# Kernel tuning notes

Hardware: AMD Instinct MI355X
Metric: run time of the kernel (lower is better)

## Reference

```python
import jax, jax.numpy as jnp
import numpy as np

DIM = 2048
HEAD = 256
SEQ = 4096

def setup_inputs() -> dict:
    key = jax.random.key(0)
    ks = jax.random.split(key, 7)
    s = 1.0 / np.sqrt(DIM)
    return {
        "marketStateBatch": jax.random.normal(ks[0], (SEQ, DIM), dtype=jnp.float32),
        "Wq": jax.random.uniform(ks[1], (HEAD, DIM), jnp.float32, -s, s),
        "bq": jax.random.uniform(ks[2], (HEAD,), jnp.float32, -s, s),
        "Wk": jax.random.uniform(ks[3], (HEAD, DIM), jnp.float32, -s, s),
        "bk": jax.random.uniform(ks[4], (HEAD,), jnp.float32, -s, s),
        "Wv": jax.random.uniform(ks[5], (HEAD, DIM), jnp.float32, -s, s),
        "bv": jax.random.uniform(ks[6], (HEAD,), jnp.float32, -s, s),
    }

def reference(marketStateBatch, Wq, bq, Wk, bk, Wv, bv):
    x = marketStateBatch  # [S, D]
    q = x @ Wq.T + bq     # [S, H]
    k = x @ Wk.T + bk     # [S, H]
    v = x @ Wv.T + bv     # [S, H]
    # NOTE: original scales by sqrt(dimensionSize), the INPUT dim, not head dim.
    scores = (q @ k.T) * (1.0 / np.sqrt(DIM))  # [S, S]
    S = x.shape[0]
    causal = jnp.tril(jnp.ones((S, S), dtype=bool))
    scores = jnp.where(causal, scores, -jnp.inf)
    attn = jax.nn.softmax(scores, axis=-1)
    # torch.nan_to_num(attn, 0.0): rows are never all -inf here (diag kept),
    # but replicate the op faithfully.
    attn = jnp.nan_to_num(attn, nan=0.0)
    return attn @ v  # [S, H]
```

## Files before the change

kernel.cpp:

```cpp
#include <hip/hip_runtime.h>
#include <stdint.h>

#define SEQ 4096
#define DIMK 2048
#define HD 256

typedef __attribute__((ext_vector_type(8))) short bf16x8;
typedef __attribute__((ext_vector_type(4))) short u16x4;
typedef __attribute__((ext_vector_type(4))) float f32x4;
typedef __attribute__((ext_vector_type(16))) float f32x16;
typedef unsigned short u16;
typedef unsigned int u32;

#define BAR() asm volatile("s_barrier" ::: "memory")
#define VMCNT(n) asm volatile("s_waitcnt vmcnt(" #n ")" ::: "memory")

__device__ __forceinline__ u16 f2bf(float f) {
    u32 u = __float_as_uint(f);
    u += 0x7FFFu + ((u >> 16) & 1u);
    return (u16)(u >> 16);
}

__device__ __forceinline__ float bf2f(u16 h) {
    u32 u = ((u32)h) << 16;
    return __uint_as_float(u);
}

__device__ __forceinline__ bf16x8 pack8(f32x4 a0, f32x4 a1) {
    bf16x8 v8;
    v8[0]=(short)f2bf(a0[0]); v8[1]=(short)f2bf(a0[1]);
    v8[2]=(short)f2bf(a0[2]); v8[3]=(short)f2bf(a0[3]);
    v8[4]=(short)f2bf(a1[0]); v8[5]=(short)f2bf(a1[1]);
    v8[6]=(short)f2bf(a1[2]); v8[7]=(short)f2bf(a1[3]);
    return v8;
}

__device__ __forceinline__ void gl16(const void* g, void* l) {
    __builtin_amdgcn_global_load_lds(
        (const __attribute__((address_space(1))) void*)g,
        (__attribute__((address_space(3))) void*)l, 16, 0, 0);
}

__device__ __forceinline__ u32 cvtpk(float lo, float hi) {
    u32 d;
    asm("v_cvt_pk_bf16_f32 %0, %1, %2" : "=v"(d) : "v"(lo), "v"(hi));
    return d;
}

__device__ __forceinline__ void plswap(u32& x, u32& y) {
#if __has_builtin(__builtin_amdgcn_permlane32_swap)
    typedef int i32x2 __attribute__((ext_vector_type(2)));
    i32x2 r = __builtin_amdgcn_permlane32_swap((int)x, (int)y, false, false);
    x = (u32)r[0]; y = (u32)r[1];
#else
    asm("v_permlane32_swap_b32 %0, %1" : "+v"(x), "+v"(y));
#endif
}

__global__ __launch_bounds__(256) void cvt_all2(
    const float* __restrict__ x, const float* __restrict__ Wq,
    const float* __restrict__ Wk, const float* __restrict__ Wv,
    u16* __restrict__ xb_sw, u16* __restrict__ wb_sw)
{
    const int y = blockIdx.y;
    int i = blockIdx.x * 256 + threadIdx.x;
    int stride = gridDim.x * 256;
    if (y == 0) {
        for (; i < SEQ*DIMK/8; i += stride) {
            int row = i >> 8, c8 = i & 255;
            f32x4 a0 = *(const f32x4*)(x + (size_t)row*DIMK + c8*8);
            f32x4 a1 = *(const f32x4*)(x + (size_t)row*DIMK + c8*8 + 4);
            int mt = row >> 6, rl = row & 63, kt = c8 >> 3, sl = c8 & 7;
            size_t dst = ((size_t)(mt*32 + kt))*4096 + rl*64 + ((sl ^ (rl&7))*8);
            *(bf16x8*)(xb_sw + dst) = pack8(a0, a1);
        }
    } else {
        const float* W = (y==1) ? Wq : (y==2) ? Wk : Wv;
        for (; i < HD*DIMK/8; i += stride) {
            int row = i >> 8, c8 = i & 255;
            f32x4 a0 = *(const f32x4*)(W + (size_t)row*DIMK + c8*8);
            f32x4 a1 = *(const f32x4*)(W + (size_t)row*DIMK + c8*8 + 4);
            int gr = (y-1)*256 + row;
            int nt = gr >> 7, rl = gr & 127, kt = c8 >> 3, sl = c8 & 7;
            size_t dst = ((size_t)(nt*32 + kt))*8192 + rl*64 + ((sl ^ (rl&7))*8);
            *(bf16x8*)(wb_sw + dst) = pack8(a0, a1);
        }
    }
}

__global__ __launch_bounds__(256, 2) void qkv_gemm2b(
    const u16* __restrict__ xb_sw, const u16* __restrict__ wb_sw,
    const float* __restrict__ bq, const float* __restrict__ bk,
    const float* __restrict__ bv,
    u16* __restrict__ qb, u16* __restrict__ kb_t, u16* __restrict__ vt_t)
{
    __shared__ char T[3][24576];

    const int tid = threadIdx.x;
    const int lane = tid & 63;
    const int w = tid >> 6;
    const int r = lane & 15, g = lane >> 4;
    const int wr = w >> 1, wc = w & 1;
    const int mt = blockIdx.x;
    const int y  = blockIdx.y;
    const int z  = y >> 1;
    const float* bias = (z==0) ? bq : (z==1) ? bk : bv;

    const u16* abase = xb_sw + (size_t)mt*32*4096;
    const u16* bbase = wb_sw + (size_t)y*32*8192;

    f32x4 zero = {0.f,0.f,0.f,0.f};
    f32x4 acc[2][4];
    #pragma unroll
    for (int m = 0; m < 2; ++m)
        #pragma unroll
        for (int n = 0; n < 4; ++n) acc[m][n] = zero;

    auto stage = [&](int b, int kt) {
        const u16* ag = abase + (size_t)kt*4096 + w*1024 + lane*8;
        const u16* bg = bbase + (size_t)kt*8192 + w*2048 + lane*8;
        char* al = T[b] + w*2048;
        char* bl = T[b] + 8192 + w*4096;
        gl16(ag,        al);
        gl16(ag + 512,  al + 1024);
        gl16(bg,        bl);
        gl16(bg + 512,  bl + 1024);
        gl16(bg + 1024, bl + 2048);
        gl16(bg + 1536, bl + 3072);
    };

    stage(0, 0);
    stage(1, 1);

    for (int kt = 0; kt < 32; ++kt) {
        if (kt < 31) { VMCNT(6); } else { VMCNT(0); }
        BAR();
        if (kt + 2 < 32) stage((kt + 2) % 3, kt + 2);
        const char* A = T[kt % 3];
        const char* B = T[kt % 3] + 8192;
        __builtin_amdgcn_s_setprio(1);
        #pragma unroll
        for (int kc = 0; kc < 2; ++kc) {
            bf16x8 af[2], bfr[4];
            #pragma unroll
            for (int m = 0; m < 2; ++m) {
                int arow = wr*32 + m*16 + r;
                af[m] = *(const bf16x8*)(A + arow*128 + (((kc*4+g) ^ (arow&7)) << 4));
            }
            #pragma unroll
            for (int n = 0; n < 4; ++n) {
                int brow = wc*64 + n*16 + r;
                bfr[n] = *(const bf16x8*)(B + brow*128 + (((kc*4+g) ^ (brow&7)) << 4));
            }
            #pragma unroll
            for (int m = 0; m < 2; ++m)
                #pragma unroll
                for (int n = 0; n < 4; ++n)
                    acc[m][n] = __builtin_amdgcn_mfma_f32_16x16x32_bf16(
                        af[m], bfr[n], acc[m][n], 0, 0, 0);
        }
        __builtin_amdgcn_s_setprio(0);
    }

    const int m0 = mt*64, n0 = y*128;
    const float qs = 0.03187936f;
    if (z == 0) {
        #pragma unroll
        for (int n = 0; n < 4; ++n) {
            int hc = (n0 + wc*64 + n*16 + r) & 255;
            float bcol = bias[hc];
            #pragma unroll
            for (int m = 0; m < 2; ++m) {
                int row0 = m0 + wr*32 + m*16 + g*4;
                #pragma unroll
                for (int j = 0; j < 4; ++j)
                    qb[(size_t)(row0+j)*HD + hc] = f2bf((acc[m][n][j] + bcol) * qs);
            }
        }
    } else if (z == 1) {
        #pragma unroll
        for (int n = 0; n < 4; ++n) {
            int hc = (n0 + wc*64 + n*16 + r) & 255;
            float bcol = bias[hc];
            #pragma unroll
            for (int m = 0; m < 2; ++m) {
                int row0 = m0 + wr*32 + m*16 + g*4;
                #pragma unroll
                for (int j = 0; j < 4; ++j) {
                    int rowj = row0 + j;
                    int t = rowj >> 5, rl = rowj & 31;
                    kb_t[(size_t)t*8192 + rl*256 + (((hc>>3) ^ (rl&7))*8) + (hc&7)]
                        = f2bf(acc[m][n][j] + bcol);
                }
            }
        }
    } else {
        #pragma unroll
        for (int n = 0; n < 4; ++n) {
            int hc = (n0 + wc*64 + n*16 + r) & 255;
            float bcol = bias[hc];
            #pragma unroll
            for (int m = 0; m < 2; ++m) {
                int kv0 = m0 + wr*32 + m*16 + g*4;
                int t = kv0 >> 5, kl = kv0 & 31;
                u16x4 pk;
                #pragma unroll
                for (int j = 0; j < 4; ++j) pk[j] = (short)f2bf(acc[m][n][j] + bcol);
                *(u16x4*)(vt_t + (size_t)t*8192 + hc*32 +
                          (((kl>>3) ^ (hc&3) ^ ((hc>>2)&3))*8) + (kl&7)) = pk;
            }
        }
    }
}

__global__ __launch_bounds__(256, 2) void attn_part9(
    const u16* __restrict__ qb, const u16* __restrict__ kb_t,
    const u16* __restrict__ vt_t,
    u16* __restrict__ po, float* __restrict__ pm, float* __restrict__ pl,
    int C)
{
    __shared__ char Kb[2][16384];
    __shared__ char Vb[2][16384];

    const int pid = blockIdx.x;
    int Q = 0, a0 = 0;
    for (int k = 0; k < 32; ++k) {
        int nsk = (4*k + 4 + C - 1) / C;
        if (pid < a0 + nsk) { Q = k; break; }
        a0 += nsk;
    }
    const int s  = pid - a0;
    const int nt = 4*Q + 4;
    const int t0 = s*C;
    const int t1 = min(t0 + C, nt);

    const int tid = threadIdx.x;
    const int L = tid & 63;
    const int w = tid >> 6;
    const int l31 = L & 31;
    const int h   = L >> 5;
    const int qg  = Q*128 + w*32 + l31;
    const int vsw = (l31 & 3) ^ ((l31 >> 2) & 3);
    const int kx  = l31 & 7;

    auto stage = [&](int t, int b) {
        const u16* kg = kb_t + (size_t)t*8192 + w*2048 + L*8;
        const u16* vg = vt_t + (size_t)t*8192 + w*2048 + L*8;
        char* kl = Kb[b] + w*4096;
        char* vl = Vb[b] + w*4096;
        #pragma unroll
        for (int i = 0; i < 4; ++i) gl16(kg + i*512, kl + i*1024);
        #pragma unroll
        for (int i = 0; i < 4; ++i) gl16(vg + i*512, vl + i*1024);
    };

    stage(t0, t0 & 1);
    if (t0 + 1 < t1) stage(t0 + 1, (t0 + 1) & 1);
    else             stage(t0,     (t0 + 1) & 1);

    bf16x8 qf[16];
    {
        const u16* qp = qb + (size_t)qg*HD + h*8;
        #pragma unroll
        for (int c = 0; c < 16; ++c) qf[c] = *(const bf16x8*)(qp + c*16);
    }

    f32x16 o[8];
    #pragma unroll
    for (int ht = 0; ht < 8; ++ht)
        #pragma unroll
        for (int e = 0; e < 16; ++e) o[ht][e] = 0.f;
    float lsum = 0.f;

    for (int t = t0; t < t1; ++t) {
        if (t + 1 < t1) { VMCNT(8); } else { VMCNT(0); }
        BAR();
        const char* K = Kb[t & 1];
        const char* V = Vb[t & 1];

        #define LDK(c) (*(const bf16x8*)(K + l31*512 + (((2*(c) + h) ^ kx) << 4)))
        f32x16 sv;
        #pragma unroll
        for (int e = 0; e < 16; ++e) sv[e] = 0.f;
        __builtin_amdgcn_s_setprio(1);
        {
            bf16x8 ka = LDK(0), kb_ = LDK(1);
            sv = __builtin_amdgcn_mfma_f32_32x32x16_bf16(ka,  qf[0],  sv, 0,0,0); ka  = LDK(2);
            sv = __builtin_amdgcn_mfma_f32_32x32x16_bf16(kb_, qf[1],  sv, 0,0,0); kb_ = LDK(3);
            sv = __builtin_amdgcn_mfma_f32_32x32x16_bf16(ka,  qf[2],  sv, 0,0,0); ka  = LDK(4);
            sv = __builtin_amdgcn_mfma_f32_32x32x16_bf16(kb_, qf[3],  sv, 0,0,0); kb_ = LDK(5);
            sv = __builtin_amdgcn_mfma_f32_32x32x16_bf16(ka,  qf[4],  sv, 0,0,0); ka  = LDK(6);
            sv = __builtin_amdgcn_mfma_f32_32x32x16_bf16(kb_, qf[5],  sv, 0,0,0); kb_ = LDK(7);
            sv = __builtin_amdgcn_mfma_f32_32x32x16_bf16(ka,  qf[6],  sv, 0,0,0); ka  = LDK(8);
            sv = __builtin_amdgcn_mfma_f32_32x32x16_bf16(kb_, qf[7],  sv, 0,0,0); kb_ = LDK(9);
            sv = __builtin_amdgcn_mfma_f32_32x32x16_bf16(ka,  qf[8],  sv, 0,0,0); ka  = LDK(10);
            sv = __builtin_amdgcn_mfma_f32_32x32x16_bf16(kb_, qf[9],  sv, 0,0,0); kb_ = LDK(11);
            sv = __builtin_amdgcn_mfma_f32_32x32x16_bf16(ka,  qf[10], sv, 0,0,0); ka  = LDK(12);
            sv = __builtin_amdgcn_mfma_f32_32x32x16_bf16(kb_, qf[11], sv, 0,0,0); kb_ = LDK(13);
            sv = __builtin_amdgcn_mfma_f32_32x32x16_bf16(ka,  qf[12], sv, 0,0,0); ka  = LDK(14);
            sv = __builtin_amdgcn_mfma_f32_32x32x16_bf16(kb_, qf[13], sv, 0,0,0); kb_ = LDK(15);
            sv = __builtin_amdgcn_mfma_f32_32x32x16_bf16(ka,  qf[14], sv, 0,0,0);
            sv = __builtin_amdgcn_mfma_f32_32x32x16_bf16(kb_, qf[15], sv, 0,0,0);
        }
        #undef LDK
        __builtin_amdgcn_s_setprio(0);

        if (t*32 + 31 > Q*128 + w*32) {
            #pragma unroll
            for (int e = 0; e < 16; ++e) {
                int kvr = (e & 3) + 8*(e >> 2) + 4*h;
                if (t*32 + kvr > qg) sv[e] = -__builtin_inff();
            }
        }

        #pragma unroll
        for (int e = 0; e < 16; ++e) sv[e] = exp2f(sv[e]);
        float r0 = ((sv[0]+sv[1])+(sv[2]+sv[3])) + ((sv[4]+sv[5])+(sv[6]+sv[7]));
        float r1 = ((sv[8]+sv[9])+(sv[10]+sv[11])) + ((sv[12]+sv[13])+(sv[14]+sv[15]));
        lsum += r0 + r1;

        __builtin_amdgcn_s_setprio(1);
        {
            union { u32 wd[4]; bf16x8 v8; } up0;
            u32 A = cvtpk(sv[0],  sv[1]),  B = cvtpk(sv[2],  sv[3]);
            u32 Cc= cvtpk(sv[4],  sv[5]),  D = cvtpk(sv[6],  sv[7]);
            plswap(A, Cc); plswap(B, D);
            up0.wd[0]=A; up0.wd[1]=B; up0.wd[2]=Cc; up0.wd[3]=D;
            #pragma unroll
            for (int ht = 0; ht < 8; ++ht) {
                bf16x8 vf0 = *(const bf16x8*)(V + (ht*32 + l31)*64 + (((h) ^ vsw) << 4));
                o[ht] = __builtin_amdgcn_mfma_f32_32x32x16_bf16(vf0, up0.v8, o[ht], 0, 0, 0);
            }
        }
        {
            union { u32 wd[4]; bf16x8 v8; } up1;
            u32 A1 = cvtpk(sv[8],  sv[9]),  B1 = cvtpk(sv[10], sv[11]);
            u32 C1 = cvtpk(sv[12], sv[13]), D1 = cvtpk(sv[14], sv[15]);
            plswap(A1, C1); plswap(B1, D1);
            up1.wd[0]=A1; up1.wd[1]=B1; up1.wd[2]=C1; up1.wd[3]=D1;
            #pragma unroll
            for (int ht = 0; ht < 8; ++ht) {
                bf16x8 vf1 = *(const bf16x8*)(V + (ht*32 + l31)*64 + (((2 + h) ^ vsw) << 4));
                o[ht] = __builtin_amdgcn_mfma_f32_32x32x16_bf16(vf1, up1.v8, o[ht], 0, 0, 0);
            }
        }
        __builtin_amdgcn_s_setprio(0);

        BAR();
        stage(min(t + 2, t1 - 1), t & 1);
    }

    VMCNT(0);

    float lrun = lsum + __shfl_xor(lsum, 32);
    if (h == 0) {
        pm[(size_t)pid*128 + w*32 + l31] = 0.f;
        pl[(size_t)pid*128 + w*32 + l31] = lrun;
    }
    u16* op = po + ((size_t)pid*128 + w*32 + l31) * 256;
    #pragma unroll
    for (int ht = 0; ht < 8; ++ht)
        #pragma unroll
        for (int j = 0; j < 8; ++j) {
            u32 pk = (u32)f2bf(o[ht][2*j]) | ((u32)f2bf(o[ht][2*j+1]) << 16);
            int hdb = ht*32 + (j & 1)*2 + (j >> 1)*8 + 4*h;
            *(u32*)(op + hdb) = pk;
        }
}

__global__ __launch_bounds__(256) void attn_combine5(
    const u16* __restrict__ po, const float* __restrict__ pm,
    const float* __restrict__ pl, float* __restrict__ out, int C)
{
    const int tid = threadIdx.x;
    const int row = blockIdx.x * 16 + (tid >> 4);
    const int cg  = tid & 15;
    const int Q   = row >> 7, rr = row & 127;
    const int nt  = 4*Q + 4;
    const int ns  = (nt + C - 1) / C;
    int pid0 = 0;
    for (int k = 0; k < Q; ++k) pid0 += (4*k + 4 + C - 1) / C;

    float M = -1e30f;
    for (int s = 0; s < ns; ++s)
        M = fmaxf(M, pm[(size_t)(pid0+s)*128 + rr]);

    float lt = 0.f;
    f32x4 acc[4];
    f32x4 zero = {0.f,0.f,0.f,0.f};
    #pragma unroll
    for (int v = 0; v < 4; ++v) acc[v] = zero;

    for (int s = 0; s < ns; ++s) {
        float ms  = pm[(size_t)(pid0+s)*128 + rr];
        float wgt = exp2f(ms - M);
        lt += wgt * pl[(size_t)(pid0+s)*128 + rr];
        const u16* p = po + ((size_t)(pid0+s)*128 + rr)*256 + cg*16;
        #pragma unroll
        for (int v = 0; v < 4; ++v) {
            u16x4 pv = *(const u16x4*)(p + v*4);
            #pragma unroll
            for (int e = 0; e < 4; ++e)
                acc[v][e] += wgt * bf2f((u16)pv[e]);
        }
    }
    float inv = 1.f / lt;
    f32x4* op = (f32x4*)(out + (size_t)row*256 + cg*16);
    #pragma unroll
    for (int v = 0; v < 4; ++v) op[v] = acc[v] * inv;
}

extern "C" void kernel_launch(void* const* d_in, const int* in_sizes, int n_in,
                              void* d_out, int out_size, void* d_ws, size_t ws_size,
                              hipStream_t stream) {
    const float* x  = (const float*)d_in[0];
    const float* Wq = (const float*)d_in[1];
    const float* bq = (const float*)d_in[2];
    const float* Wk = (const float*)d_in[3];
    const float* bk = (const float*)d_in[4];
    const float* Wv = (const float*)d_in[5];
    const float* bv = (const float*)d_in[6];
    float* out = (float*)d_out;

    const size_t xb_bytes  = (size_t)SEQ * DIMK * 2;
    const size_t wb_bytes  = (size_t)768 * DIMK * 2;
    const size_t qkv_bytes = (size_t)SEQ * HD * 2;
    const size_t base = xb_bytes + wb_bytes + 3*qkv_bytes;

    int C = 64;
    size_t npid = 0;
    const int cand[4] = {5, 8, 16, 64};
    for (int ci = 0; ci < 4; ++ci) {
        int c = cand[ci];
        size_t np = 0;
        for (int k = 0; k < 32; ++k) np += (size_t)(4*k + 4 + c - 1) / c;
        size_t need = base + np * ((size_t)128*256*2 + 2*128*4);
        if (need <= ws_size) { C = c; npid = np; break; }
        if (ci == 3) { C = c; npid = np; }
    }

    char* p = (char*)d_ws;
    u16* xb_sw = (u16*)p; p += xb_bytes;
    u16* wb_sw = (u16*)p; p += wb_bytes;
    u16* qbuf  = (u16*)p; p += qkv_bytes;
    u16* kb_t  = (u16*)p; p += qkv_bytes;
    u16* vt_t  = (u16*)p; p += qkv_bytes;
    u16* po    = (u16*)p; p += npid * 128 * 256 * 2;
    float* pm  = (float*)p; p += npid * 128 * 4;
    float* pl  = (float*)p; p += npid * 128 * 4;

    cvt_all2<<<dim3(512, 4), 256, 0, stream>>>(x, Wq, Wk, Wv, xb_sw, wb_sw);

    qkv_gemm2b<<<dim3(SEQ/64, 6), 256, 0, stream>>>(
        xb_sw, wb_sw, bq, bk, bv, qbuf, kb_t, vt_t);

    attn_part9<<<(int)npid, 256, 0, stream>>>(
        qbuf, kb_t, vt_t, po, pm, pl, C);

    attn_combine5<<<SEQ/16, 256, 0, stream>>>(po, pm, pl, out, C);
}
```

Measured before the change: 76.74 us.

## Software-pipeline QK^T of tile t with PV of tile t-1 in attention

Restructures the attention partial kernel so each iteration interleaves the QK^T MFMAs for the current K tile with the PV MFMAs for the previous tile's probabilities, with a prologue and an epilogue tile. K and V staging are split so that V for a tile lands one iteration later than K. The aim is to hide the dependency from score compute through exp and bf16 packing before PV can start, keeping the matrix units busy. It costs extra registers for the carried probabilities and makes the buffer and wait-count bookkeeping more intricate, which may hurt occupancy at two blocks per CU.

```diff
diff --git a/kernel.cpp b/kernel.cpp
--- a/kernel.cpp
+++ b/kernel.cpp
@@ -213,7 +213,7 @@
     }
 }
 
-__global__ __launch_bounds__(256, 2) void attn_part9(
+__global__ __launch_bounds__(256, 2) void attn_part10(
     const u16* __restrict__ qb, const u16* __restrict__ kb_t,
     const u16* __restrict__ vt_t,
     u16* __restrict__ po, float* __restrict__ pm, float* __restrict__ pl,
@@ -243,20 +243,22 @@
     const int vsw = (l31 & 3) ^ ((l31 >> 2) & 3);
     const int kx  = l31 & 7;
 
-    auto stage = [&](int t, int b) {
+    auto stageK = [&](int t, int b) {
         const u16* kg = kb_t + (size_t)t*8192 + w*2048 + L*8;
+        char* kl = Kb[b] + w*4096;
+        #pragma unroll
+        for (int i = 0; i < 4; ++i) gl16(kg + i*512, kl + i*1024);
+    };
+    auto stageV = [&](int t, int b) {
         const u16* vg = vt_t + (size_t)t*8192 + w*2048 + L*8;
-        char* kl = Kb[b] + w*4096;
         char* vl = Vb[b] + w*4096;
-        #pragma unroll
-        for (int i = 0; i < 4; ++i) gl16(kg + i*512, kl + i*1024);
         #pragma unroll
         for (int i = 0; i < 4; ++i) gl16(vg + i*512, vl + i*1024);
     };
 
-    stage(t0, t0 & 1);
-    if (t0 + 1 < t1) stage(t0 + 1, (t0 + 1) & 1);
-    else             stage(t0,     (t0 + 1) & 1);
+    stageK(t0, t0 & 1);
+    stageK(min(t0 + 1, t1 - 1), (t0 + 1) & 1);
+    stageV(t0, t0 & 1);
 
     bf16x8 qf[16];
     {
@@ -271,40 +273,9 @@
         #pragma unroll
         for (int e = 0; e < 16; ++e) o[ht][e] = 0.f;
     float lsum = 0.f;
-
-    for (int t = t0; t < t1; ++t) {
-        if (t + 1 < t1) { VMCNT(8); } else { VMCNT(0); }
-        BAR();
-        const char* K = Kb[t & 1];
-        const char* V = Vb[t & 1];
-
-        #define LDK(c) (*(const bf16x8*)(K + l31*512 + (((2*(c) + h) ^ kx) << 4)))
-        f32x16 sv;
-        #pragma unroll
-        for (int e = 0; e < 16; ++e) sv[e] = 0.f;
-        __builtin_amdgcn_s_setprio(1);
-        {
-            bf16x8 ka = LDK(0), kb_ = LDK(1);
-            sv = __builtin_amdgcn_mfma_f32_32x32x16_bf16(ka,  qf[0],  sv, 0,0,0); ka  = LDK(2);
-            sv = __builtin_amdgcn_mfma_f32_32x32x16_bf16(kb_, qf[1],  sv, 0,0,0); kb_ = LDK(3);
-            sv = __builtin_amdgcn_mfma_f32_32x32x16_bf16(ka,  qf[2],  sv, 0,0,0); ka  = LDK(4);
-            sv = __builtin_amdgcn_mfma_f32_32x32x16_bf16(kb_, qf[3],  sv, 0,0,0); kb_ = LDK(5);
-            sv = __builtin_amdgcn_mfma_f32_32x32x16_bf16(ka,  qf[4],  sv, 0,0,0); ka  = LDK(6);
-            sv = __builtin_amdgcn_mfma_f32_32x32x16_bf16(kb_, qf[5],  sv, 0,0,0); kb_ = LDK(7);
-            sv = __builtin_amdgcn_mfma_f32_32x32x16_bf16(ka,  qf[6],  sv, 0,0,0); ka  = LDK(8);
-            sv = __builtin_amdgcn_mfma_f32_32x32x16_bf16(kb_, qf[7],  sv, 0,0,0); kb_ = LDK(9);
-            sv = __builtin_amdgcn_mfma_f32_32x32x16_bf16(ka,  qf[8],  sv, 0,0,0); ka  = LDK(10);
-            sv = __builtin_amdgcn_mfma_f32_32x32x16_bf16(kb_, qf[9],  sv, 0,0,0); kb_ = LDK(11);
-            sv = __builtin_amdgcn_mfma_f32_32x32x16_bf16(ka,  qf[10], sv, 0,0,0); ka  = LDK(12);
-            sv = __builtin_amdgcn_mfma_f32_32x32x16_bf16(kb_, qf[11], sv, 0,0,0); kb_ = LDK(13);
-            sv = __builtin_amdgcn_mfma_f32_32x32x16_bf16(ka,  qf[12], sv, 0,0,0); ka  = LDK(14);
-            sv = __builtin_amdgcn_mfma_f32_32x32x16_bf16(kb_, qf[13], sv, 0,0,0); kb_ = LDK(15);
-            sv = __builtin_amdgcn_mfma_f32_32x32x16_bf16(ka,  qf[14], sv, 0,0,0);
-            sv = __builtin_amdgcn_mfma_f32_32x32x16_bf16(kb_, qf[15], sv, 0,0,0);
-        }
-        #undef LDK
-        __builtin_amdgcn_s_setprio(0);
-
+    bf16x8 pp0, pp1;
+
+    auto finish_tile = [&](f32x16& sv, int t) {
         if (t*32 + 31 > Q*128 + w*32) {
             #pragma unroll
             for (int e = 0; e < 16; ++e) {
@@ -312,45 +283,106 @@
                 if (t*32 + kvr > qg) sv[e] = -__builtin_inff();
             }
         }
-
         #pragma unroll
         for (int e = 0; e < 16; ++e) sv[e] = exp2f(sv[e]);
         float r0 = ((sv[0]+sv[1])+(sv[2]+sv[3])) + ((sv[4]+sv[5])+(sv[6]+sv[7]));
         float r1 = ((sv[8]+sv[9])+(sv[10]+sv[11])) + ((sv[12]+sv[13])+(sv[14]+sv[15]));
         lsum += r0 + r1;
-
-        __builtin_amdgcn_s_setprio(1);
         {
-            union { u32 wd[4]; bf16x8 v8; } up0;
+            union { u32 wd[4]; bf16x8 v8; } up;
             u32 A = cvtpk(sv[0],  sv[1]),  B = cvtpk(sv[2],  sv[3]);
             u32 Cc= cvtpk(sv[4],  sv[5]),  D = cvtpk(sv[6],  sv[7]);
             plswap(A, Cc); plswap(B, D);
-            up0.wd[0]=A; up0.wd[1]=B; up0.wd[2]=Cc; up0.wd[3]=D;
-            #pragma unroll
-            for (int ht = 0; ht < 8; ++ht) {
-                bf16x8 vf0 = *(const bf16x8*)(V + (ht*32 + l31)*64 + (((h) ^ vsw) << 4));
-                o[ht] = __builtin_amdgcn_mfma_f32_32x32x16_bf16(vf0, up0.v8, o[ht], 0, 0, 0);
-            }
+            up.wd[0]=A; up.wd[1]=B; up.wd[2]=Cc; up.wd[3]=D;
+            pp0 = up.v8;
         }
         {
-            union { u32 wd[4]; bf16x8 v8; } up1;
+            union { u32 wd[4]; bf16x8 v8; } up;
             u32 A1 = cvtpk(sv[8],  sv[9]),  B1 = cvtpk(sv[10], sv[11]);
             u32 C1 = cvtpk(sv[12], sv[13]), D1 = cvtpk(sv[14], sv[15]);
             plswap(A1, C1); plswap(B1, D1);
-            up1.wd[0]=A1; up1.wd[1]=B1; up1.wd[2]=C1; up1.wd[3]=D1;
-            #pragma unroll
-            for (int ht = 0; ht < 8; ++ht) {
-                bf16x8 vf1 = *(const bf16x8*)(V + (ht*32 + l31)*64 + (((2 + h) ^ vsw) << 4));
-                o[ht] = __builtin_amdgcn_mfma_f32_32x32x16_bf16(vf1, up1.v8, o[ht], 0, 0, 0);
-            }
-        }
+            up.wd[0]=A1; up.wd[1]=B1; up.wd[2]=C1; up.wd[3]=D1;
+            pp1 = up.v8;
+        }
+    };
+
+    {
+        VMCNT(8);
+        BAR();
+        const char* K = Kb[t0 & 1];
+        #define LDK(c) (*(const bf16x8*)(K + l31*512 + (((2*(c) + h) ^ kx) << 4)))
+        f32x16 sv;
+        #pragma unroll
+        for (int e = 0; e < 16; ++e) sv[e] = 0.f;
+        __builtin_amdgcn_s_setprio(1);
+        {
+            bf16x8 kk0 = LDK(0), kk1 = LDK(1);
+            #pragma unroll
+            for (int c = 0; c < 16; ++c) {
+                bf16x8 kc = (c & 1) ? kk1 : kk0;
+                sv = __builtin_amdgcn_mfma_f32_32x32x16_bf16(kc, qf[c], sv, 0, 0, 0);
+                if (c + 2 < 16) { if (c & 1) kk1 = LDK(c + 2); else kk0 = LDK(c + 2); }
+            }
+        }
+        #undef LDK
         __builtin_amdgcn_s_setprio(0);
-
+        finish_tile(sv, t0);
         BAR();
-        stage(min(t + 2, t1 - 1), t & 1);
+        stageK(min(t0 + 2, t1 - 1), t0 & 1);
+        stageV(min(t0 + 1, t1 - 1), (t0 + 1) & 1);
+    }
+
+    for (int t = t0 + 1; t < t1; ++t) {
+        VMCNT(8);
+        BAR();
+        const char* K  = Kb[t & 1];
+        const char* Vp = Vb[(t - 1) & 1];
+
+        #define LDK(c) (*(const bf16x8*)(K + l31*512 + (((2*(c) + h) ^ kx) << 4)))
+        f32x16 sv;
+        #pragma unroll
+        for (int e = 0; e < 16; ++e) sv[e] = 0.f;
+        __builtin_amdgcn_s_setprio(1);
+        {
+            bf16x8 kk0 = LDK(0), kk1 = LDK(1);
+            #pragma unroll
+            for (int c = 0; c < 16; ++c) {
+                bf16x8 kc = (c & 1) ? kk1 : kk0;
+                sv = __builtin_amdgcn_mfma_f32_32x32x16_bf16(kc, qf[c], sv, 0, 0, 0);
+                if (c + 2 < 16) { if (c & 1) kk1 = LDK(c + 2); else kk0 = LDK(c + 2); }
+                {
+                    const int ht = c & 7;
+                    const int sl = ((c < 8) ? h : (2 + h)) ^ vsw;
+                    bf16x8 vf = *(const bf16x8*)(Vp + (ht*32 + l31)*64 + (sl << 4));
+                    o[ht] = __builtin_amdgcn_mfma_f32_32x32x16_bf16(
+                        vf, (c < 8) ? pp0 : pp1, o[ht], 0, 0, 0);
+                }
+            }
+        }
+        #undef LDK
+        __builtin_amdgcn_s_setprio(0);
+
+        finish_tile(sv, t);
+
+        BAR();
+        stageK(min(t + 2, t1 - 1), t & 1);
+        stageV(min(t + 1, t1 - 1), (t + 1) & 1);
     }
 
     VMCNT(0);
+    BAR();
+    {
+        const char* Vp = Vb[(t1 - 1) & 1];
+        __builtin_amdgcn_s_setprio(1);
+        #pragma unroll
+        for (int ht = 0; ht < 8; ++ht) {
+            bf16x8 vf0 = *(const bf16x8*)(Vp + (ht*32 + l31)*64 + (((h)     ^ vsw) << 4));
+            bf16x8 vf1 = *(const bf16x8*)(Vp + (ht*32 + l31)*64 + (((2 + h) ^ vsw) << 4));
+            o[ht] = __builtin_amdgcn_mfma_f32_32x32x16_bf16(vf0, pp0, o[ht], 0, 0, 0);
+            o[ht] = __builtin_amdgcn_mfma_f32_32x32x16_bf16(vf1, pp1, o[ht], 0, 0, 0);
+        }
+        __builtin_amdgcn_s_setprio(0);
+    }
 
     float lrun = lsum + __shfl_xor(lsum, 32);
     if (h == 0) {
@@ -454,7 +486,7 @@
     qkv_gemm2b<<<dim3(SEQ/64, 6), 256, 0, stream>>>(
         xb_sw, wb_sw, bq, bk, bv, qbuf, kb_t, vt_t);
 
-    attn_part9<<<(int)npid, 256, 0, stream>>>(
+    attn_part10<<<(int)npid, 256, 0, stream>>>(
         qbuf, kb_t, vt_t, po, pm, pl, C);
 
     attn_combine5<<<SEQ/16, 256, 0, stream>>>(po, pm, pl, out, C);
```

After: 75.94 us (median of 3 runs). Within noise of the previous version (-1.0%).

## Read V fragments directly from global memory and interleave block order

Applied to the files above, without the earlier changes.

Removes the LDS staging of V tiles, so each wave loads its V fragments straight from global memory (relying on cache), which halves shared memory use and the async copy traffic per step. The block index is remapped to alternate between the front and back of the partition list, mixing heavy and light causal work across the launch. The K MFMA chain is also rewritten as an unrolled loop. The risk is higher global-load latency exposed in the PV loop, since those loads are not prefetched.

```diff
diff --git a/kernel.cpp b/kernel.cpp
--- a/kernel.cpp
+++ b/kernel.cpp
@@ -213,16 +213,18 @@
     }
 }
 
-__global__ __launch_bounds__(256, 2) void attn_part9(
+__global__ __launch_bounds__(256, 2) void attn_part11(
     const u16* __restrict__ qb, const u16* __restrict__ kb_t,
     const u16* __restrict__ vt_t,
     u16* __restrict__ po, float* __restrict__ pm, float* __restrict__ pl,
     int C)
 {
     __shared__ char Kb[2][16384];
-    __shared__ char Vb[2][16384];
-
-    const int pid = blockIdx.x;
+
+    const int nb  = (int)gridDim.x;
+    const int bid = blockIdx.x;
+    const int pid = (bid & 1) ? (nb - 1 - (bid >> 1)) : (bid >> 1);
+
     int Q = 0, a0 = 0;
     for (int k = 0; k < 32; ++k) {
         int nsk = (4*k + 4 + C - 1) / C;
@@ -243,20 +245,15 @@
     const int vsw = (l31 & 3) ^ ((l31 >> 2) & 3);
     const int kx  = l31 & 7;
 
-    auto stage = [&](int t, int b) {
+    auto stageK = [&](int t, int b) {
         const u16* kg = kb_t + (size_t)t*8192 + w*2048 + L*8;
-        const u16* vg = vt_t + (size_t)t*8192 + w*2048 + L*8;
         char* kl = Kb[b] + w*4096;
-        char* vl = Vb[b] + w*4096;
         #pragma unroll
         for (int i = 0; i < 4; ++i) gl16(kg + i*512, kl + i*1024);
-        #pragma unroll
-        for (int i = 0; i < 4; ++i) gl16(vg + i*512, vl + i*1024);
     };
 
-    stage(t0, t0 & 1);
-    if (t0 + 1 < t1) stage(t0 + 1, (t0 + 1) & 1);
-    else             stage(t0,     (t0 + 1) & 1);
+    stageK(t0, t0 & 1);
+    stageK(min(t0 + 1, t1 - 1), (t0 + 1) & 1);
 
     bf16x8 qf[16];
     {
@@ -273,10 +270,10 @@
     float lsum = 0.f;
 
     for (int t = t0; t < t1; ++t) {
-        if (t + 1 < t1) { VMCNT(8); } else { VMCNT(0); }
+        if (t + 1 < t1) { VMCNT(4); } else { VMCNT(0); }
         BAR();
-        const char* K = Kb[t & 1];
-        const char* V = Vb[t & 1];
+        const char* K  = Kb[t & 1];
+        const char* Vg = (const char*)vt_t + (size_t)t*16384;
 
         #define LDK(c) (*(const bf16x8*)(K + l31*512 + (((2*(c) + h) ^ kx) << 4)))
         f32x16 sv;
@@ -285,22 +282,12 @@
         __builtin_amdgcn_s_setprio(1);
         {
             bf16x8 ka = LDK(0), kb_ = LDK(1);
-            sv = __builtin_amdgcn_mfma_f32_32x32x16_bf16(ka,  qf[0],  sv, 0,0,0); ka  = LDK(2);
-            sv = __builtin_amdgcn_mfma_f32_32x32x16_bf16(kb_, qf[1],  sv, 0,0,0); kb_ = LDK(3);
-            sv = __builtin_amdgcn_mfma_f32_32x32x16_bf16(ka,  qf[2],  sv, 0,0,0); ka  = LDK(4);
-            sv = __builtin_amdgcn_mfma_f32_32x32x16_bf16(kb_, qf[3],  sv, 0,0,0); kb_ = LDK(5);
-            sv = __builtin_amdgcn_mfma_f32_32x32x16_bf16(ka,  qf[4],  sv, 0,0,0); ka  = LDK(6);
-            sv = __builtin_amdgcn_mfma_f32_32x32x16_bf16(kb_, qf[5],  sv, 0,0,0); kb_ = LDK(7);
-            sv = __builtin_amdgcn_mfma_f32_32x32x16_bf16(ka,  qf[6],  sv, 0,0,0); ka  = LDK(8);
-            sv = __builtin_amdgcn_mfma_f32_32x32x16_bf16(kb_, qf[7],  sv, 0,0,0); kb_ = LDK(9);
-            sv = __builtin_amdgcn_mfma_f32_32x32x16_bf16(ka,  qf[8],  sv, 0,0,0); ka  = LDK(10);
-            sv = __builtin_amdgcn_mfma_f32_32x32x16_bf16(kb_, qf[9],  sv, 0,0,0); kb_ = LDK(11);
-            sv = __builtin_amdgcn_mfma_f32_32x32x16_bf16(ka,  qf[10], sv, 0,0,0); ka  = LDK(12);
-            sv = __builtin_amdgcn_mfma_f32_32x32x16_bf16(kb_, qf[11], sv, 0,0,0); kb_ = LDK(13);
-            sv = __builtin_amdgcn_mfma_f32_32x32x16_bf16(ka,  qf[12], sv, 0,0,0); ka  = LDK(14);
-            sv = __builtin_amdgcn_mfma_f32_32x32x16_bf16(kb_, qf[13], sv, 0,0,0); kb_ = LDK(15);
-            sv = __builtin_amdgcn_mfma_f32_32x32x16_bf16(ka,  qf[14], sv, 0,0,0);
-            sv = __builtin_amdgcn_mfma_f32_32x32x16_bf16(kb_, qf[15], sv, 0,0,0);
+            #pragma unroll
+            for (int c = 0; c < 16; ++c) {
+                bf16x8 kc = (c & 1) ? kb_ : ka;
+                sv = __builtin_amdgcn_mfma_f32_32x32x16_bf16(kc, qf[c], sv, 0, 0, 0);
+                if (c + 2 < 16) { if (c & 1) kb_ = LDK(c + 2); else ka = LDK(c + 2); }
+            }
         }
         #undef LDK
         __builtin_amdgcn_s_setprio(0);
@@ -328,7 +315,7 @@
             up0.wd[0]=A; up0.wd[1]=B; up0.wd[2]=Cc; up0.wd[3]=D;
             #pragma unroll
             for (int ht = 0; ht < 8; ++ht) {
-                bf16x8 vf0 = *(const bf16x8*)(V + (ht*32 + l31)*64 + (((h) ^ vsw) << 4));
+                bf16x8 vf0 = *(const bf16x8*)(Vg + (ht*32 + l31)*64 + (((h) ^ vsw) << 4));
                 o[ht] = __builtin_amdgcn_mfma_f32_32x32x16_bf16(vf0, up0.v8, o[ht], 0, 0, 0);
             }
         }
@@ -340,14 +327,14 @@
             up1.wd[0]=A1; up1.wd[1]=B1; up1.wd[2]=C1; up1.wd[3]=D1;
             #pragma unroll
             for (int ht = 0; ht < 8; ++ht) {
-                bf16x8 vf1 = *(const bf16x8*)(V + (ht*32 + l31)*64 + (((2 + h) ^ vsw) << 4));
+                bf16x8 vf1 = *(const bf16x8*)(Vg + (ht*32 + l31)*64 + (((2 + h) ^ vsw) << 4));
                 o[ht] = __builtin_amdgcn_mfma_f32_32x32x16_bf16(vf1, up1.v8, o[ht], 0, 0, 0);
             }
         }
         __builtin_amdgcn_s_setprio(0);
 
         BAR();
-        stage(min(t + 2, t1 - 1), t & 1);
+        stageK(min(t + 2, t1 - 1), t & 1);
     }
 
     VMCNT(0);
@@ -454,7 +441,7 @@
     qkv_gemm2b<<<dim3(SEQ/64, 6), 256, 0, stream>>>(
         xb_sw, wb_sw, bq, bk, bv, qbuf, kb_t, vt_t);
 
-    attn_part9<<<(int)npid, 256, 0, stream>>>(
+    attn_part11<<<(int)npid, 256, 0, stream>>>(
         qbuf, kb_t, vt_t, po, pm, pl, C);
 
     attn_combine5<<<SEQ/16, 256, 0, stream>>>(po, pm, pl, out, C);
```

Result: slower. 87.33 us (+13.8%).
